# Kernel tuning notes

Hardware: AMD Instinct MI355X
Metric: run time of the kernel (lower is better)

Reference implementation:

```python
import jax, jax.numpy as jnp
import numpy as np

N_NODES = 100000
N_EDGES = 1600000
D_IN = 64


def _graph_conv(x, edge_src, edge_dst, W, b, n_nodes):
    # gather source features along edges, mean-aggregate at destinations,
    # then linear transform + ReLU (standard GraphConv semantics)
    msgs = x[edge_src]  # [E, d]
    agg = jax.ops.segment_sum(msgs, edge_dst, num_segments=n_nodes)  # [N, d]
    deg = jax.ops.segment_sum(jnp.ones((edge_src.shape[0],), x.dtype), edge_dst,
                              num_segments=n_nodes)  # [N]
    agg = agg / jnp.maximum(deg, 1.0)[:, None]
    return jax.nn.relu(agg @ W + b)


def setup_inputs() -> dict:
    key = jax.random.key(0)
    ks = jax.random.split(key, 6)
    node_features = jax.random.normal(ks[0], (N_NODES, D_IN), dtype=jnp.float32)
    edge_src = jax.random.randint(ks[1], (N_EDGES,), 0, N_NODES)
    edge_dst = jax.random.randint(ks[2], (N_EDGES,), 0, N_NODES)
    W1 = jax.random.normal(ks[3], (D_IN, 64), dtype=jnp.float32) * (1.0 / np.sqrt(D_IN))
    b1 = jnp.zeros((64,), jnp.float32)
    W2 = jax.random.normal(ks[4], (64, 32), dtype=jnp.float32) * (1.0 / np.sqrt(64))
    b2 = jnp.zeros((32,), jnp.float32)
    Wd = jax.random.normal(ks[5], (1, 1), dtype=jnp.float32)
    bd = jnp.zeros((1,), jnp.float32)
    return {"node_features": node_features, "edge_src": edge_src, "edge_dst": edge_dst,
            "W1": W1, "b1": b1, "W2": W2, "b2": b2, "Wd": Wd, "bd": bd}


def reference(node_features, edge_src, edge_dst, W1, b1, W2, b2, Wd, bd):
    n_nodes = node_features.shape[0]
    x = _graph_conv(node_features, edge_src, edge_dst, W1, b1, n_nodes)  # [N, 64]
    x = _graph_conv(x, edge_src, edge_dst, W2, b2, n_nodes)              # [N, 32]
    x = jnp.mean(x, axis=1, keepdims=True)                               # [N, 1]
    return jax.nn.sigmoid(x @ Wd + bd)                                   # [N, 1]
```

## Files before the change

### kernel.cpp

```cpp
#include <hip/hip_runtime.h>
#include <hip/hip_bf16.h>

#define N_NODES 100000
#define N_EDGES 1600000
#define N_PAD   100096
#define BSHIFT  7
#define NBUCKET 782
#define BCAP    3072
#define EPB     2048

__device__ __forceinline__ unsigned short f32_to_bf16(float f) {
    unsigned int u = __float_as_uint(f);
    unsigned int r = (u + 0x7fffu + ((u >> 16) & 1u)) >> 16;
    return (unsigned short)r;
}
__device__ __forceinline__ float bf16_lo(unsigned int p) {
    return __uint_as_float(p << 16);
}
__device__ __forceinline__ float bf16_hi(unsigned int p) {
    return __uint_as_float(p & 0xffff0000u);
}

__global__ void __launch_bounds__(256) bucket_scatter_lds(
    const int* __restrict__ src, const int* __restrict__ dst,
    int* __restrict__ bcur, unsigned int* __restrict__ tmp, int n_edges) {
    __shared__ int lh[1024];
    int t = threadIdx.x;
    int e0 = blockIdx.x * EPB;
    int e1 = min(e0 + EPB, n_edges);
    for (int i = t; i < 1024; i += 256) lh[i] = 0;
    __syncthreads();
    for (int e = e0 + t; e < e1; e += 256)
        atomicAdd(&lh[dst[e] >> BSHIFT], 1);
    __syncthreads();
    for (int i = t; i < NBUCKET; i += 256) {
        int c = lh[i];
        lh[i] = (c > 0) ? atomicAdd(&bcur[i], c) : 0;
    }
    __syncthreads();
    for (int e = e0 + t; e < e1; e += 256) {
        int s = src[e], d = dst[e];
        int b = d >> BSHIFT;
        int p = atomicAdd(&lh[b], 1);
        if (p < BCAP)
            tmp[(size_t)b * BCAP + p] = ((unsigned)s << BSHIFT) | (unsigned)(d & 127);
    }
}

__global__ void __launch_bounds__(256) bucket_to_csr(
    const unsigned int* __restrict__ tmp, const int* __restrict__ bcur,
    int* __restrict__ row_ptr, int* __restrict__ cnt,
    int* __restrict__ col, int n_nodes) {
    __shared__ int nh[128];
    __shared__ int npref[128];
    int b = blockIdx.x;
    int t = threadIdx.x;
    int m = min(bcur[b], BCAP);
    int cbase = b * BCAP;
    if (t < 128) nh[t] = 0;
    __syncthreads();
    const unsigned int* te = tmp + (size_t)b * BCAP;
    for (int i = t; i < m; i += 256) atomicAdd(&nh[te[i] & 127], 1);
    __syncthreads();
    if (t < 128) npref[t] = nh[t];
    __syncthreads();
    for (int off = 1; off < 128; off <<= 1) {
        int u = (t < 128 && t >= off) ? npref[t - off] : 0;
        __syncthreads();
        if (t < 128) npref[t] += u;
        __syncthreads();
    }
    if (t < 128) {
        int node = (b << BSHIFT) + t;
        int ex = npref[t] - nh[t];
        if (node < n_nodes) { row_ptr[node] = cbase + ex; cnt[node] = nh[t]; }
        nh[t] = cbase + ex;
    }
    __syncthreads();
    for (int i = t; i < m; i += 256) {
        unsigned int e = te[i];
        int pos = atomicAdd(&nh[e & 127], 1);
        col[pos] = (int)(e >> BSHIFT);
    }
}

__global__ void __launch_bounds__(256) gemm_n64(const float4* __restrict__ X4,
                                                const float* __restrict__ W,
                                                unsigned short* __restrict__ Y, int M) {
    __shared__ float sx[64][65];
    __shared__ float sw[64 * 64];
    int t = threadIdx.x;
    int base = blockIdx.x * 64;
    for (int i = t; i < 64 * 16; i += 256) {
        int r = i >> 4, c4 = i & 15;
        int row = base + r;
        float4 v = make_float4(0.f, 0.f, 0.f, 0.f);
        if (row < M) v = X4[(size_t)row * 16 + c4];
        sx[r][c4 * 4 + 0] = v.x; sx[r][c4 * 4 + 1] = v.y;
        sx[r][c4 * 4 + 2] = v.z; sx[r][c4 * 4 + 3] = v.w;
    }
    float4* sw4 = (float4*)sw;
    const float4* W4 = (const float4*)W;
    for (int i = t; i < 64 * 16; i += 256) sw4[i] = W4[i];
    __syncthreads();

    int tm = t & 15;
    int tn = t >> 4;
    float acc[4][4] = {{0.f}};
    #pragma unroll 8
    for (int k = 0; k < 64; k++) {
        float4 b = sw4[k * 16 + tn];
        float a0 = sx[tm * 4 + 0][k], a1 = sx[tm * 4 + 1][k];
        float a2 = sx[tm * 4 + 2][k], a3 = sx[tm * 4 + 3][k];
        acc[0][0] = fmaf(a0, b.x, acc[0][0]); acc[0][1] = fmaf(a0, b.y, acc[0][1]);
        acc[0][2] = fmaf(a0, b.z, acc[0][2]); acc[0][3] = fmaf(a0, b.w, acc[0][3]);
        acc[1][0] = fmaf(a1, b.x, acc[1][0]); acc[1][1] = fmaf(a1, b.y, acc[1][1]);
        acc[1][2] = fmaf(a1, b.z, acc[1][2]); acc[1][3] = fmaf(a1, b.w, acc[1][3]);
        acc[2][0] = fmaf(a2, b.x, acc[2][0]); acc[2][1] = fmaf(a2, b.y, acc[2][1]);
        acc[2][2] = fmaf(a2, b.z, acc[2][2]); acc[2][3] = fmaf(a2, b.w, acc[2][3]);
        acc[3][0] = fmaf(a3, b.x, acc[3][0]); acc[3][1] = fmaf(a3, b.y, acc[3][1]);
        acc[3][2] = fmaf(a3, b.z, acc[3][2]); acc[3][3] = fmaf(a3, b.w, acc[3][3]);
    }
    #pragma unroll
    for (int i = 0; i < 4; i++) {
        int row = base + tm * 4 + i;
        if (row < M) {
            ushort4 p;
            p.x = f32_to_bf16(acc[i][0]); p.y = f32_to_bf16(acc[i][1]);
            p.z = f32_to_bf16(acc[i][2]); p.w = f32_to_bf16(acc[i][3]);
            *(ushort4*)&Y[(size_t)row * 64 + tn * 4] = p;
        }
    }
}

__global__ void __launch_bounds__(256) gemm_n32(const float4* __restrict__ X4,
                                                const float* __restrict__ W,
                                                unsigned short* __restrict__ Z, int M) {
    __shared__ float sx[128][65];
    __shared__ float sw[64 * 32];
    int t = threadIdx.x;
    int base = blockIdx.x * 128;
    for (int i = t; i < 128 * 16; i += 256) {
        int r = i >> 4, c4 = i & 15;
        int row = base + r;
        float4 v = make_float4(0.f, 0.f, 0.f, 0.f);
        if (row < M) v = X4[(size_t)row * 16 + c4];
        sx[r][c4 * 4 + 0] = v.x; sx[r][c4 * 4 + 1] = v.y;
        sx[r][c4 * 4 + 2] = v.z; sx[r][c4 * 4 + 3] = v.w;
    }
    float4* sw4 = (float4*)sw;
    const float4* W4 = (const float4*)W;
    for (int i = t; i < 64 * 8; i += 256) sw4[i] = W4[i];
    __syncthreads();

    int tm = t & 31;
    int tn = t >> 5;
    float acc[4][4] = {{0.f}};
    #pragma unroll 8
    for (int k = 0; k < 64; k++) {
        float4 b = sw4[k * 8 + tn];
        float a0 = sx[tm * 4 + 0][k], a1 = sx[tm * 4 + 1][k];
        float a2 = sx[tm * 4 + 2][k], a3 = sx[tm * 4 + 3][k];
        acc[0][0] = fmaf(a0, b.x, acc[0][0]); acc[0][1] = fmaf(a0, b.y, acc[0][1]);
        acc[0][2] = fmaf(a0, b.z, acc[0][2]); acc[0][3] = fmaf(a0, b.w, acc[0][3]);
        acc[1][0] = fmaf(a1, b.x, acc[1][0]); acc[1][1] = fmaf(a1, b.y, acc[1][1]);
        acc[1][2] = fmaf(a1, b.z, acc[1][2]); acc[1][3] = fmaf(a1, b.w, acc[1][3]);
        acc[2][0] = fmaf(a2, b.x, acc[2][0]); acc[2][1] = fmaf(a2, b.y, acc[2][1]);
        acc[2][2] = fmaf(a2, b.z, acc[2][2]); acc[2][3] = fmaf(a2, b.w, acc[2][3]);
        acc[3][0] = fmaf(a3, b.x, acc[3][0]); acc[3][1] = fmaf(a3, b.y, acc[3][1]);
        acc[3][2] = fmaf(a3, b.z, acc[3][2]); acc[3][3] = fmaf(a3, b.w, acc[3][3]);
    }
    #pragma unroll
    for (int i = 0; i < 4; i++) {
        int row = base + tm * 4 + i;
        if (row < M) {
            ushort4 p;
            p.x = f32_to_bf16(acc[i][0]); p.y = f32_to_bf16(acc[i][1]);
            p.z = f32_to_bf16(acc[i][2]); p.w = f32_to_bf16(acc[i][3]);
            *(ushort4*)&Z[(size_t)row * 32 + tn * 4] = p;
        }
    }
}

__global__ void __launch_bounds__(256) gather_relu64(
    const uint4* __restrict__ Y4, const int* __restrict__ row_ptr,
    const int* __restrict__ col, const int* __restrict__ cnt,
    const float* __restrict__ b1, float4* __restrict__ H4, int n_nodes) {
    int n = blockIdx.x * 4 + (threadIdx.x >> 6);
    if (n >= n_nodes) return;
    int lane = threadIdx.x & 63;
    int g = lane >> 3;
    int c = lane & 7;
    int beg = row_ptr[n];
    int d = cnt[n];

    float acc[8] = {0.f, 0.f, 0.f, 0.f, 0.f, 0.f, 0.f, 0.f};
    for (int i = 0; i < d; i += 8) {
        int idx = i + g;
        if (idx < d) {
            int s = col[beg + idx];
            uint4 v = Y4[(size_t)s * 8 + c];
            acc[0] += bf16_lo(v.x); acc[1] += bf16_hi(v.x);
            acc[2] += bf16_lo(v.y); acc[3] += bf16_hi(v.y);
            acc[4] += bf16_lo(v.z); acc[5] += bf16_hi(v.z);
            acc[6] += bf16_lo(v.w); acc[7] += bf16_hi(v.w);
        }
    }
    #pragma unroll
    for (int m = 8; m <= 32; m <<= 1) {
        #pragma unroll
        for (int q = 0; q < 8; q++) acc[q] += __shfl_xor(acc[q], m);
    }
    float inv = 1.0f / fmaxf((float)d, 1.0f);
    const float4* b1_4 = (const float4*)b1;
    float4 ba = b1_4[c * 2], bb = b1_4[c * 2 + 1];
    if (g == 0) {
        float4 o0, o1;
        o0.x = fmaxf(fmaf(acc[0], inv, ba.x), 0.f);
        o0.y = fmaxf(fmaf(acc[1], inv, ba.y), 0.f);
        o0.z = fmaxf(fmaf(acc[2], inv, ba.z), 0.f);
        o0.w = fmaxf(fmaf(acc[3], inv, ba.w), 0.f);
        o1.x = fmaxf(fmaf(acc[4], inv, bb.x), 0.f);
        o1.y = fmaxf(fmaf(acc[5], inv, bb.y), 0.f);
        o1.z = fmaxf(fmaf(acc[6], inv, bb.z), 0.f);
        o1.w = fmaxf(fmaf(acc[7], inv, bb.w), 0.f);
        H4[(size_t)n * 16 + c * 2]     = o0;
        H4[(size_t)n * 16 + c * 2 + 1] = o1;
    }
}

__global__ void __launch_bounds__(256) gather_final32(
    const uint4* __restrict__ Z4, const int* __restrict__ row_ptr,
    const int* __restrict__ col, const int* __restrict__ cnt,
    const float* __restrict__ b2, const float* __restrict__ Wd,
    const float* __restrict__ bd, float* __restrict__ out, int n_nodes) {
    int n = blockIdx.x * 4 + (threadIdx.x >> 6);
    if (n >= n_nodes) return;
    int lane = threadIdx.x & 63;
    int g = lane >> 2;
    int c = lane & 3;
    int beg = row_ptr[n];
    int d = cnt[n];

    float acc[8] = {0.f, 0.f, 0.f, 0.f, 0.f, 0.f, 0.f, 0.f};
    for (int i = 0; i < d; i += 16) {
        int idx = i + g;
        if (idx < d) {
            int s = col[beg + idx];
            uint4 v = Z4[(size_t)s * 4 + c];
            acc[0] += bf16_lo(v.x); acc[1] += bf16_hi(v.x);
            acc[2] += bf16_lo(v.y); acc[3] += bf16_hi(v.y);
            acc[4] += bf16_lo(v.z); acc[5] += bf16_hi(v.z);
            acc[6] += bf16_lo(v.w); acc[7] += bf16_hi(v.w);
        }
    }
    #pragma unroll
    for (int m = 4; m <= 32; m <<= 1) {
        #pragma unroll
        for (int q = 0; q < 8; q++) acc[q] += __shfl_xor(acc[q], m);
    }
    float inv = 1.0f / fmaxf((float)d, 1.0f);
    const float4* b2_4 = (const float4*)b2;
    float4 ba = b2_4[c * 2], bb = b2_4[c * 2 + 1];
    float local = 0.f;
    local += fmaxf(fmaf(acc[0], inv, ba.x), 0.f);
    local += fmaxf(fmaf(acc[1], inv, ba.y), 0.f);
    local += fmaxf(fmaf(acc[2], inv, ba.z), 0.f);
    local += fmaxf(fmaf(acc[3], inv, ba.w), 0.f);
    local += fmaxf(fmaf(acc[4], inv, bb.x), 0.f);
    local += fmaxf(fmaf(acc[5], inv, bb.y), 0.f);
    local += fmaxf(fmaf(acc[6], inv, bb.z), 0.f);
    local += fmaxf(fmaf(acc[7], inv, bb.w), 0.f);
    local += __shfl_xor(local, 1);
    local += __shfl_xor(local, 2);
    if (lane == 0) {
        float z = fmaf(local * (1.0f / 32.0f), Wd[0], bd[0]);
        out[n] = 1.0f / (1.0f + __expf(-z));
    }
}

extern "C" void kernel_launch(void* const* d_in, const int* in_sizes, int n_in,
                              void* d_out, int out_size, void* d_ws, size_t ws_size,
                              hipStream_t stream) {
    const float* x    = (const float*)d_in[0];
    const int*   esrc = (const int*)d_in[1];
    const int*   edst = (const int*)d_in[2];
    const float* W1   = (const float*)d_in[3];
    const float* b1   = (const float*)d_in[4];
    const float* W2   = (const float*)d_in[5];
    const float* b2   = (const float*)d_in[6];
    const float* Wd   = (const float*)d_in[7];
    const float* bd   = (const float*)d_in[8];
    float* out = (float*)d_out;

    int* bcur    = (int*)d_ws;
    int* row_ptr = bcur + 1024;
    int* cnt     = row_ptr + N_PAD;
    int* col     = cnt + N_PAD;
    float* h     = (float*)(col + (size_t)NBUCKET * BCAP);
    unsigned int* tmp = (unsigned int*)h;
    unsigned short* y  = (unsigned short*)(h + (size_t)N_NODES * 64);
    unsigned short* z2 = y;

    hipMemsetAsync((void*)bcur, 0, 1024 * sizeof(int), stream);

    bucket_scatter_lds<<<(N_EDGES + EPB - 1) / EPB, 256, 0, stream>>>(
        esrc, edst, bcur, tmp, N_EDGES);
    bucket_to_csr<<<NBUCKET, 256, 0, stream>>>(tmp, bcur, row_ptr, cnt, col, N_NODES);

    gemm_n64<<<(N_NODES + 63) / 64, 256, 0, stream>>>((const float4*)x, W1, y, N_NODES);
    gather_relu64<<<(N_NODES + 3) / 4, 256, 0, stream>>>(
        (const uint4*)y, row_ptr, col, cnt, b1, (float4*)h, N_NODES);
    gemm_n32<<<(N_NODES + 127) / 128, 256, 0, stream>>>((const float4*)h, W2, z2, N_NODES);
    gather_final32<<<(N_NODES + 3) / 4, 256, 0, stream>>>(
        (const uint4*)z2, row_ptr, col, cnt, b2, Wd, bd, out, N_NODES);
}
```

Baseline: 266.3 us.

## Store GEMM outputs in 16-feature column panels and gather panel by panel

The GEMM kernels now write bf16 features into separate column panels of 16 features per node rather than contiguous rows. The gather kernels iterate over panels, accumulating each panel across all neighbors before moving to the next, so the random-access working set per pass is smaller and more likely to stay cache resident. The trade-off is re-reading the edge index list once per panel, narrower per-lane loads, and extra loop and shuffle-reduction overhead.

```diff
diff --git a/kernel.cpp b/kernel.cpp
--- a/kernel.cpp
+++ b/kernel.cpp
@@ -121,6 +121,8 @@
         acc[3][0] = fmaf(a3, b.x, acc[3][0]); acc[3][1] = fmaf(a3, b.y, acc[3][1]);
         acc[3][2] = fmaf(a3, b.z, acc[3][2]); acc[3][3] = fmaf(a3, b.w, acc[3][3]);
     }
+    int q = tn >> 2, cc = tn & 3;
+    size_t pbase = (size_t)q * N_NODES;
     #pragma unroll
     for (int i = 0; i < 4; i++) {
         int row = base + tm * 4 + i;
@@ -128,7 +130,7 @@
             ushort4 p;
             p.x = f32_to_bf16(acc[i][0]); p.y = f32_to_bf16(acc[i][1]);
             p.z = f32_to_bf16(acc[i][2]); p.w = f32_to_bf16(acc[i][3]);
-            *(ushort4*)&Y[(size_t)row * 64 + tn * 4] = p;
+            *(ushort4*)&Y[(pbase + row) * 16 + cc * 4] = p;
         }
     }
 }
@@ -170,6 +172,8 @@
         acc[3][0] = fmaf(a3, b.x, acc[3][0]); acc[3][1] = fmaf(a3, b.y, acc[3][1]);
         acc[3][2] = fmaf(a3, b.z, acc[3][2]); acc[3][3] = fmaf(a3, b.w, acc[3][3]);
     }
+    int q = tn >> 2, cc = tn & 3;
+    size_t pbase = (size_t)q * N_NODES;
     #pragma unroll
     for (int i = 0; i < 4; i++) {
         int row = base + tm * 4 + i;
@@ -177,60 +181,54 @@
             ushort4 p;
             p.x = f32_to_bf16(acc[i][0]); p.y = f32_to_bf16(acc[i][1]);
             p.z = f32_to_bf16(acc[i][2]); p.w = f32_to_bf16(acc[i][3]);
-            *(ushort4*)&Z[(size_t)row * 32 + tn * 4] = p;
+            *(ushort4*)&Z[(pbase + row) * 16 + cc * 4] = p;
         }
     }
 }
 
 __global__ void __launch_bounds__(256) gather_relu64(
-    const uint4* __restrict__ Y4, const int* __restrict__ row_ptr,
+    const uint2* __restrict__ Y2, const int* __restrict__ row_ptr,
     const int* __restrict__ col, const int* __restrict__ cnt,
     const float* __restrict__ b1, float4* __restrict__ H4, int n_nodes) {
     int n = blockIdx.x * 4 + (threadIdx.x >> 6);
     if (n >= n_nodes) return;
     int lane = threadIdx.x & 63;
-    int g = lane >> 3;
-    int c = lane & 7;
+    int g = lane >> 2;
+    int c = lane & 3;
     int beg = row_ptr[n];
     int d = cnt[n];
-
-    float acc[8] = {0.f, 0.f, 0.f, 0.f, 0.f, 0.f, 0.f, 0.f};
-    for (int i = 0; i < d; i += 8) {
-        int idx = i + g;
-        if (idx < d) {
-            int s = col[beg + idx];
-            uint4 v = Y4[(size_t)s * 8 + c];
-            acc[0] += bf16_lo(v.x); acc[1] += bf16_hi(v.x);
-            acc[2] += bf16_lo(v.y); acc[3] += bf16_hi(v.y);
-            acc[4] += bf16_lo(v.z); acc[5] += bf16_hi(v.z);
-            acc[6] += bf16_lo(v.w); acc[7] += bf16_hi(v.w);
-        }
-    }
-    #pragma unroll
-    for (int m = 8; m <= 32; m <<= 1) {
-        #pragma unroll
-        for (int q = 0; q < 8; q++) acc[q] += __shfl_xor(acc[q], m);
-    }
     float inv = 1.0f / fmaxf((float)d, 1.0f);
     const float4* b1_4 = (const float4*)b1;
-    float4 ba = b1_4[c * 2], bb = b1_4[c * 2 + 1];
-    if (g == 0) {
-        float4 o0, o1;
-        o0.x = fmaxf(fmaf(acc[0], inv, ba.x), 0.f);
-        o0.y = fmaxf(fmaf(acc[1], inv, ba.y), 0.f);
-        o0.z = fmaxf(fmaf(acc[2], inv, ba.z), 0.f);
-        o0.w = fmaxf(fmaf(acc[3], inv, ba.w), 0.f);
-        o1.x = fmaxf(fmaf(acc[4], inv, bb.x), 0.f);
-        o1.y = fmaxf(fmaf(acc[5], inv, bb.y), 0.f);
-        o1.z = fmaxf(fmaf(acc[6], inv, bb.z), 0.f);
-        o1.w = fmaxf(fmaf(acc[7], inv, bb.w), 0.f);
-        H4[(size_t)n * 16 + c * 2]     = o0;
-        H4[(size_t)n * 16 + c * 2 + 1] = o1;
+
+    #pragma unroll
+    for (int q = 0; q < 4; q++) {
+        size_t pbase = (size_t)q * N_NODES;
+        float a0 = 0.f, a1 = 0.f, a2 = 0.f, a3 = 0.f;
+        for (int i = g; i < d; i += 16) {
+            int s = col[beg + i];
+            uint2 v = Y2[(pbase + s) * 4 + c];
+            a0 += bf16_lo(v.x); a1 += bf16_hi(v.x);
+            a2 += bf16_lo(v.y); a3 += bf16_hi(v.y);
+        }
+        #pragma unroll
+        for (int m = 4; m <= 32; m <<= 1) {
+            a0 += __shfl_xor(a0, m); a1 += __shfl_xor(a1, m);
+            a2 += __shfl_xor(a2, m); a3 += __shfl_xor(a3, m);
+        }
+        if (g == 0) {
+            float4 bb = b1_4[q * 4 + c];
+            float4 o;
+            o.x = fmaxf(fmaf(a0, inv, bb.x), 0.f);
+            o.y = fmaxf(fmaf(a1, inv, bb.y), 0.f);
+            o.z = fmaxf(fmaf(a2, inv, bb.z), 0.f);
+            o.w = fmaxf(fmaf(a3, inv, bb.w), 0.f);
+            H4[(size_t)n * 16 + q * 4 + c] = o;
+        }
     }
 }
 
 __global__ void __launch_bounds__(256) gather_final32(
-    const uint4* __restrict__ Z4, const int* __restrict__ row_ptr,
+    const uint2* __restrict__ Z2, const int* __restrict__ row_ptr,
     const int* __restrict__ col, const int* __restrict__ cnt,
     const float* __restrict__ b2, const float* __restrict__ Wd,
     const float* __restrict__ bd, float* __restrict__ out, int n_nodes) {
@@ -241,36 +239,33 @@
     int c = lane & 3;
     int beg = row_ptr[n];
     int d = cnt[n];
-
-    float acc[8] = {0.f, 0.f, 0.f, 0.f, 0.f, 0.f, 0.f, 0.f};
-    for (int i = 0; i < d; i += 16) {
-        int idx = i + g;
-        if (idx < d) {
-            int s = col[beg + idx];
-            uint4 v = Z4[(size_t)s * 4 + c];
-            acc[0] += bf16_lo(v.x); acc[1] += bf16_hi(v.x);
-            acc[2] += bf16_lo(v.y); acc[3] += bf16_hi(v.y);
-            acc[4] += bf16_lo(v.z); acc[5] += bf16_hi(v.z);
-            acc[6] += bf16_lo(v.w); acc[7] += bf16_hi(v.w);
-        }
-    }
-    #pragma unroll
-    for (int m = 4; m <= 32; m <<= 1) {
-        #pragma unroll
-        for (int q = 0; q < 8; q++) acc[q] += __shfl_xor(acc[q], m);
-    }
     float inv = 1.0f / fmaxf((float)d, 1.0f);
     const float4* b2_4 = (const float4*)b2;
-    float4 ba = b2_4[c * 2], bb = b2_4[c * 2 + 1];
     float local = 0.f;
-    local += fmaxf(fmaf(acc[0], inv, ba.x), 0.f);
-    local += fmaxf(fmaf(acc[1], inv, ba.y), 0.f);
-    local += fmaxf(fmaf(acc[2], inv, ba.z), 0.f);
-    local += fmaxf(fmaf(acc[3], inv, ba.w), 0.f);
-    local += fmaxf(fmaf(acc[4], inv, bb.x), 0.f);
-    local += fmaxf(fmaf(acc[5], inv, bb.y), 0.f);
-    local += fmaxf(fmaf(acc[6], inv, bb.z), 0.f);
-    local += fmaxf(fmaf(acc[7], inv, bb.w), 0.f);
+
+    #pragma unroll
+    for (int q = 0; q < 2; q++) {
+        size_t pbase = (size_t)q * N_NODES;
+        float a0 = 0.f, a1 = 0.f, a2 = 0.f, a3 = 0.f;
+        for (int i = g; i < d; i += 16) {
+            int s = col[beg + i];
+            uint2 v = Z2[(pbase + s) * 4 + c];
+            a0 += bf16_lo(v.x); a1 += bf16_hi(v.x);
+            a2 += bf16_lo(v.y); a3 += bf16_hi(v.y);
+        }
+        #pragma unroll
+        for (int m = 4; m <= 32; m <<= 1) {
+            a0 += __shfl_xor(a0, m); a1 += __shfl_xor(a1, m);
+            a2 += __shfl_xor(a2, m); a3 += __shfl_xor(a3, m);
+        }
+        if (g == 0) {
+            float4 bb = b2_4[q * 4 + c];
+            local += fmaxf(fmaf(a0, inv, bb.x), 0.f);
+            local += fmaxf(fmaf(a1, inv, bb.y), 0.f);
+            local += fmaxf(fmaf(a2, inv, bb.z), 0.f);
+            local += fmaxf(fmaf(a3, inv, bb.w), 0.f);
+        }
+    }
     local += __shfl_xor(local, 1);
     local += __shfl_xor(local, 2);
     if (lane == 0) {
@@ -310,8 +305,8 @@
 
     gemm_n64<<<(N_NODES + 63) / 64, 256, 0, stream>>>((const float4*)x, W1, y, N_NODES);
     gather_relu64<<<(N_NODES + 3) / 4, 256, 0, stream>>>(
-        (const uint4*)y, row_ptr, col, cnt, b1, (float4*)h, N_NODES);
+        (const uint2*)y, row_ptr, col, cnt, b1, (float4*)h, N_NODES);
     gemm_n32<<<(N_NODES + 127) / 128, 256, 0, stream>>>((const float4*)h, W2, z2, N_NODES);
     gather_final32<<<(N_NODES + 3) / 4, 256, 0, stream>>>(
-        (const uint4*)z2, row_ptr, col, cnt, b2, Wd, bd, out, N_NODES);
-}
+        (const uint2*)z2, row_ptr, col, cnt, b2, Wd, bd, out, N_NODES);
+}
```

Result: slower. 334.2 us (+25.5%).

## Fuse second-layer GEMM into first gather as per-node GEMV

Applied to the files above, without the earlier changes.

The layer-1 gather now applies bias and ReLU, then multiplies the 64-wide hidden row by W2 inside the same wavefront using register-held W2 slices and shuffle reductions. It writes the 32-wide bf16 z2 directly, which removes the fp32 hidden buffer round trip and the separate gemm_n32 launch. The gather loops also drop the inner bounds check by starting at the lane's group index. In exchange each wavefront holds 32 extra registers of W2 and does redundant FMAs across lanes, which may lower occupancy in the latency-bound gather.

```diff
diff --git a/kernel.cpp b/kernel.cpp
--- a/kernel.cpp
+++ b/kernel.cpp
@@ -133,59 +133,11 @@
     }
 }
 
-__global__ void __launch_bounds__(256) gemm_n32(const float4* __restrict__ X4,
-                                                const float* __restrict__ W,
-                                                unsigned short* __restrict__ Z, int M) {
-    __shared__ float sx[128][65];
-    __shared__ float sw[64 * 32];
-    int t = threadIdx.x;
-    int base = blockIdx.x * 128;
-    for (int i = t; i < 128 * 16; i += 256) {
-        int r = i >> 4, c4 = i & 15;
-        int row = base + r;
-        float4 v = make_float4(0.f, 0.f, 0.f, 0.f);
-        if (row < M) v = X4[(size_t)row * 16 + c4];
-        sx[r][c4 * 4 + 0] = v.x; sx[r][c4 * 4 + 1] = v.y;
-        sx[r][c4 * 4 + 2] = v.z; sx[r][c4 * 4 + 3] = v.w;
-    }
-    float4* sw4 = (float4*)sw;
-    const float4* W4 = (const float4*)W;
-    for (int i = t; i < 64 * 8; i += 256) sw4[i] = W4[i];
-    __syncthreads();
-
-    int tm = t & 31;
-    int tn = t >> 5;
-    float acc[4][4] = {{0.f}};
-    #pragma unroll 8
-    for (int k = 0; k < 64; k++) {
-        float4 b = sw4[k * 8 + tn];
-        float a0 = sx[tm * 4 + 0][k], a1 = sx[tm * 4 + 1][k];
-        float a2 = sx[tm * 4 + 2][k], a3 = sx[tm * 4 + 3][k];
-        acc[0][0] = fmaf(a0, b.x, acc[0][0]); acc[0][1] = fmaf(a0, b.y, acc[0][1]);
-        acc[0][2] = fmaf(a0, b.z, acc[0][2]); acc[0][3] = fmaf(a0, b.w, acc[0][3]);
-        acc[1][0] = fmaf(a1, b.x, acc[1][0]); acc[1][1] = fmaf(a1, b.y, acc[1][1]);
-        acc[1][2] = fmaf(a1, b.z, acc[1][2]); acc[1][3] = fmaf(a1, b.w, acc[1][3]);
-        acc[2][0] = fmaf(a2, b.x, acc[2][0]); acc[2][1] = fmaf(a2, b.y, acc[2][1]);
-        acc[2][2] = fmaf(a2, b.z, acc[2][2]); acc[2][3] = fmaf(a2, b.w, acc[2][3]);
-        acc[3][0] = fmaf(a3, b.x, acc[3][0]); acc[3][1] = fmaf(a3, b.y, acc[3][1]);
-        acc[3][2] = fmaf(a3, b.z, acc[3][2]); acc[3][3] = fmaf(a3, b.w, acc[3][3]);
-    }
-    #pragma unroll
-    for (int i = 0; i < 4; i++) {
-        int row = base + tm * 4 + i;
-        if (row < M) {
-            ushort4 p;
-            p.x = f32_to_bf16(acc[i][0]); p.y = f32_to_bf16(acc[i][1]);
-            p.z = f32_to_bf16(acc[i][2]); p.w = f32_to_bf16(acc[i][3]);
-            *(ushort4*)&Z[(size_t)row * 32 + tn * 4] = p;
-        }
-    }
-}
-
-__global__ void __launch_bounds__(256) gather_relu64(
+__global__ void __launch_bounds__(256) gather_gemv(
     const uint4* __restrict__ Y4, const int* __restrict__ row_ptr,
     const int* __restrict__ col, const int* __restrict__ cnt,
-    const float* __restrict__ b1, float4* __restrict__ H4, int n_nodes) {
+    const float* __restrict__ b1, const float* __restrict__ W2,
+    unsigned short* __restrict__ z2, int n_nodes) {
     int n = blockIdx.x * 4 + (threadIdx.x >> 6);
     if (n >= n_nodes) return;
     int lane = threadIdx.x & 63;
@@ -194,17 +146,19 @@
     int beg = row_ptr[n];
     int d = cnt[n];
 
+    float4 w2v[8];
+    #pragma unroll
+    for (int q = 0; q < 8; q++)
+        w2v[q] = *(const float4*)&W2[(8 * c + q) * 32 + 4 * g];
+
     float acc[8] = {0.f, 0.f, 0.f, 0.f, 0.f, 0.f, 0.f, 0.f};
-    for (int i = 0; i < d; i += 8) {
-        int idx = i + g;
-        if (idx < d) {
-            int s = col[beg + idx];
-            uint4 v = Y4[(size_t)s * 8 + c];
-            acc[0] += bf16_lo(v.x); acc[1] += bf16_hi(v.x);
-            acc[2] += bf16_lo(v.y); acc[3] += bf16_hi(v.y);
-            acc[4] += bf16_lo(v.z); acc[5] += bf16_hi(v.z);
-            acc[6] += bf16_lo(v.w); acc[7] += bf16_hi(v.w);
-        }
+    for (int i = g; i < d; i += 8) {
+        int s = col[beg + i];
+        uint4 v = Y4[(size_t)s * 8 + c];
+        acc[0] += bf16_lo(v.x); acc[1] += bf16_hi(v.x);
+        acc[2] += bf16_lo(v.y); acc[3] += bf16_hi(v.y);
+        acc[4] += bf16_lo(v.z); acc[5] += bf16_hi(v.z);
+        acc[6] += bf16_lo(v.w); acc[7] += bf16_hi(v.w);
     }
     #pragma unroll
     for (int m = 8; m <= 32; m <<= 1) {
@@ -214,18 +168,33 @@
     float inv = 1.0f / fmaxf((float)d, 1.0f);
     const float4* b1_4 = (const float4*)b1;
     float4 ba = b1_4[c * 2], bb = b1_4[c * 2 + 1];
-    if (g == 0) {
-        float4 o0, o1;
-        o0.x = fmaxf(fmaf(acc[0], inv, ba.x), 0.f);
-        o0.y = fmaxf(fmaf(acc[1], inv, ba.y), 0.f);
-        o0.z = fmaxf(fmaf(acc[2], inv, ba.z), 0.f);
-        o0.w = fmaxf(fmaf(acc[3], inv, ba.w), 0.f);
-        o1.x = fmaxf(fmaf(acc[4], inv, bb.x), 0.f);
-        o1.y = fmaxf(fmaf(acc[5], inv, bb.y), 0.f);
-        o1.z = fmaxf(fmaf(acc[6], inv, bb.z), 0.f);
-        o1.w = fmaxf(fmaf(acc[7], inv, bb.w), 0.f);
-        H4[(size_t)n * 16 + c * 2]     = o0;
-        H4[(size_t)n * 16 + c * 2 + 1] = o1;
+    float hq[8];
+    hq[0] = fmaxf(fmaf(acc[0], inv, ba.x), 0.f);
+    hq[1] = fmaxf(fmaf(acc[1], inv, ba.y), 0.f);
+    hq[2] = fmaxf(fmaf(acc[2], inv, ba.z), 0.f);
+    hq[3] = fmaxf(fmaf(acc[3], inv, ba.w), 0.f);
+    hq[4] = fmaxf(fmaf(acc[4], inv, bb.x), 0.f);
+    hq[5] = fmaxf(fmaf(acc[5], inv, bb.y), 0.f);
+    hq[6] = fmaxf(fmaf(acc[6], inv, bb.z), 0.f);
+    hq[7] = fmaxf(fmaf(acc[7], inv, bb.w), 0.f);
+    float z0 = 0.f, z1 = 0.f, z2v = 0.f, z3 = 0.f;
+    #pragma unroll
+    for (int q = 0; q < 8; q++) {
+        z0 = fmaf(hq[q], w2v[q].x, z0);
+        z1 = fmaf(hq[q], w2v[q].y, z1);
+        z2v = fmaf(hq[q], w2v[q].z, z2v);
+        z3 = fmaf(hq[q], w2v[q].w, z3);
+    }
+    #pragma unroll
+    for (int m = 1; m <= 4; m <<= 1) {
+        z0 += __shfl_xor(z0, m); z1 += __shfl_xor(z1, m);
+        z2v += __shfl_xor(z2v, m); z3 += __shfl_xor(z3, m);
+    }
+    if (c == 0) {
+        ushort4 p;
+        p.x = f32_to_bf16(z0); p.y = f32_to_bf16(z1);
+        p.z = f32_to_bf16(z2v); p.w = f32_to_bf16(z3);
+        *(ushort4*)&z2[(size_t)n * 32 + g * 4] = p;
     }
 }
 
@@ -243,16 +212,13 @@
     int d = cnt[n];
 
     float acc[8] = {0.f, 0.f, 0.f, 0.f, 0.f, 0.f, 0.f, 0.f};
-    for (int i = 0; i < d; i += 16) {
-        int idx = i + g;
-        if (idx < d) {
-            int s = col[beg + idx];
-            uint4 v = Z4[(size_t)s * 4 + c];
-            acc[0] += bf16_lo(v.x); acc[1] += bf16_hi(v.x);
-            acc[2] += bf16_lo(v.y); acc[3] += bf16_hi(v.y);
-            acc[4] += bf16_lo(v.z); acc[5] += bf16_hi(v.z);
-            acc[6] += bf16_lo(v.w); acc[7] += bf16_hi(v.w);
-        }
+    for (int i = g; i < d; i += 16) {
+        int s = col[beg + i];
+        uint4 v = Z4[(size_t)s * 4 + c];
+        acc[0] += bf16_lo(v.x); acc[1] += bf16_hi(v.x);
+        acc[2] += bf16_lo(v.y); acc[3] += bf16_hi(v.y);
+        acc[4] += bf16_lo(v.z); acc[5] += bf16_hi(v.z);
+        acc[6] += bf16_lo(v.w); acc[7] += bf16_hi(v.w);
     }
     #pragma unroll
     for (int m = 4; m <= 32; m <<= 1) {
@@ -297,10 +263,9 @@
     int* row_ptr = bcur + 1024;
     int* cnt     = row_ptr + N_PAD;
     int* col     = cnt + N_PAD;
-    float* h     = (float*)(col + (size_t)NBUCKET * BCAP);
-    unsigned int* tmp = (unsigned int*)h;
-    unsigned short* y  = (unsigned short*)(h + (size_t)N_NODES * 64);
-    unsigned short* z2 = y;
+    unsigned int* tmp  = (unsigned int*)(col + (size_t)NBUCKET * BCAP);
+    unsigned short* y  = (unsigned short*)(tmp + (size_t)NBUCKET * BCAP);
+    unsigned short* z2 = y + (size_t)N_NODES * 64;
 
     hipMemsetAsync((void*)bcur, 0, 1024 * sizeof(int), stream);
 
@@ -309,9 +274,8 @@
     bucket_to_csr<<<NBUCKET, 256, 0, stream>>>(tmp, bcur, row_ptr, cnt, col, N_NODES);
 
     gemm_n64<<<(N_NODES + 63) / 64, 256, 0, stream>>>((const float4*)x, W1, y, N_NODES);
-    gather_relu64<<<(N_NODES + 3) / 4, 256, 0, stream>>>(
-        (const uint4*)y, row_ptr, col, cnt, b1, (float4*)h, N_NODES);
-    gemm_n32<<<(N_NODES + 127) / 128, 256, 0, stream>>>((const float4*)h, W2, z2, N_NODES);
+    gather_gemv<<<(N_NODES + 3) / 4, 256, 0, stream>>>(
+        (const uint4*)y, row_ptr, col, cnt, b1, W2, z2, N_NODES);
     gather_final32<<<(N_NODES + 3) / 4, 256, 0, stream>>>(
         (const uint4*)z2, row_ptr, col, cnt, b2, Wd, bd, out, N_NODES);
 }
```

Result: slower. 312.4 us (+17.3%).
